# Kernel tuning notes

Hardware: AMD Instinct MI355X
Metric: run time of the kernel (lower is better)

Reference implementation:

```python
import jax, jax.numpy as jnp
import numpy as np

# dims: batch, seq, input_dim, excellence_dim, heads, n_experts, top_k
B, S, D, E, H, NE, K = 4, 256, 1024, 2048, 16, 4, 2
HD = E // H  # 128


def _ln(x, g, b, eps=1e-5):
    m = jnp.mean(x, -1, keepdims=True)
    v = jnp.mean((x - m) ** 2, -1, keepdims=True)
    return (x - m) / jnp.sqrt(v + eps) * g + b


def _mlp2(x, w1, b1, w2, b2):
    # Linear -> ReLU -> Linear (torch Linear convention: y = x @ W.T + b)
    return jnp.maximum(x @ w1.T + b1, 0.0) @ w2.T + b2


def _mha(h, in_w, in_b, out_w, out_b):
    # h: (B,S,E); fused qkv in_proj like nn.MultiheadAttention
    qkv = h @ in_w.T + in_b
    q, k, v = jnp.split(qkv, 3, axis=-1)
    sp = lambda t: t.reshape(B, S, H, HD).transpose(0, 2, 1, 3)  # (B,H,S,HD)
    q, k, v = sp(q), sp(k), sp(v)
    att = jax.nn.softmax(jnp.einsum('bhqd,bhkd->bhqk', q, k) / np.float32(np.sqrt(HD)), axis=-1)
    o = jnp.einsum('bhqk,bhkd->bhqd', att, v).transpose(0, 2, 1, 3).reshape(B, S, E)
    return o @ out_w.T + out_b


def _lstm(x, w_ih, w_hh, b_ih, b_hh):
    # single-layer LSTM, torch gate order i,f,g,o. x: (B,S,E)
    pre = jnp.einsum('bsd,gd->bsg', x, w_ih) + b_ih + b_hh  # (B,S,4E)

    def step(carry, p):
        h, c = carry
        g = p + h @ w_hh.T
        i, f, gg, o = jnp.split(g, 4, axis=-1)
        c = jax.nn.sigmoid(f) * c + jax.nn.sigmoid(i) * jnp.tanh(gg)
        h = jax.nn.sigmoid(o) * jnp.tanh(c)
        return (h, c), h

    h0 = jnp.zeros((x.shape[0], E), x.dtype)
    _, hs = jax.lax.scan(step, (h0, h0), pre.transpose(1, 0, 2))
    return hs.transpose(1, 0, 2)  # (B,S,E)


def _expert(p, x):
    h = _ln(_mlp2(x, p['enc_w1'], p['enc_b1'], p['enc_w2'], p['enc_b2']), p['enc_ln_g'], p['enc_ln_b'])
    a = _mha(h, p['attn_in_w'], p['attn_in_b'], p['attn_out_w'], p['attn_out_b'])
    m = _lstm(a, p['lstm_w_ih'], p['lstm_w_hh'], p['lstm_b_ih'], p['lstm_b_hh'])
    exc = jax.nn.sigmoid(_mlp2(m, p['exc_w1'], p['exc_b1'], p['exc_w2'], p['exc_b2']))
    opt = jnp.tanh(_mlp2(m, p['opt_w1'], p['opt_b1'], p['opt_w2'], p['opt_b2']))
    return _ln(_mlp2(exc * opt, p['dec_w1'], p['dec_b1'], p['dec_w2'], p['dec_b2']), p['dec_ln_g'], p['dec_ln_b'])


_PNAMES = ['enc_w1', 'enc_b1', 'enc_w2', 'enc_b2', 'enc_ln_g', 'enc_ln_b', 'attn_in_w', 'attn_in_b', 'attn_out_w', 'attn_out_b', 'lstm_w_ih', 'lstm_w_hh', 'lstm_b_ih', 'lstm_b_hh', 'exc_w1', 'exc_b1', 'exc_w2', 'exc_b2', 'opt_w1', 'opt_b1', 'opt_w2', 'opt_b2', 'dec_w1', 'dec_b1', 'dec_w2', 'dec_b2', 'dec_ln_g', 'dec_ln_b']


def _forward(x, gate_w, gate_b, *ep):
    p = dict(zip(_PNAMES, ep))  # each leaf has leading expert axis NE
    pooled = x.mean(axis=1)  # (B,D)
    probs = jax.nn.softmax(pooled @ gate_w + gate_b, axis=-1)  # (B,NE)
    vals, idx = jax.lax.top_k(probs, K)
    vals = vals / jnp.sum(vals, -1, keepdims=True)
    w = jnp.zeros((B, NE), x.dtype).at[jnp.arange(B)[:, None], idx].set(vals)
    outs = jax.vmap(lambda pe: _expert(pe, x))(p)  # (NE,B,S,D)
    return jnp.einsum('ebsd,be->bsd', outs, w)


def setup_inputs() -> dict:
    ks = iter(jax.random.split(jax.random.key(0), 40))
    w = lambda *s: jax.random.normal(next(ks), s, jnp.float32) * 0.02
    z = lambda *s: jnp.zeros(s, jnp.float32)
    o = lambda *s: jnp.ones(s, jnp.float32)
    return {
        'x': jax.random.normal(next(ks), (B, S, D), jnp.float32),
        'gate_w': w(D, NE), 'gate_b': z(NE),
        'enc_w1': w(NE, E, D), 'enc_b1': z(NE, E), 'enc_w2': w(NE, E, E), 'enc_b2': z(NE, E),
        'enc_ln_g': o(NE, E), 'enc_ln_b': z(NE, E),
        'attn_in_w': w(NE, 3 * E, E), 'attn_in_b': z(NE, 3 * E),
        'attn_out_w': w(NE, E, E), 'attn_out_b': z(NE, E),
        'lstm_w_ih': w(NE, 4 * E, E), 'lstm_w_hh': w(NE, 4 * E, E),
        'lstm_b_ih': z(NE, 4 * E), 'lstm_b_hh': z(NE, 4 * E),
        'exc_w1': w(NE, E, E), 'exc_b1': z(NE, E), 'exc_w2': w(NE, E, E), 'exc_b2': z(NE, E),
        'opt_w1': w(NE, E, E), 'opt_b1': z(NE, E), 'opt_w2': w(NE, E, E), 'opt_b2': z(NE, E),
        'dec_w1': w(NE, E, E), 'dec_b1': z(NE, E), 'dec_w2': w(NE, D, E), 'dec_b2': z(NE, D),
        'dec_ln_g': o(NE, D), 'dec_ln_b': z(NE, D),
    }


def reference(x, gate_w, gate_b, enc_w1, enc_b1, enc_w2, enc_b2, enc_ln_g, enc_ln_b, attn_in_w, attn_in_b, attn_out_w, attn_out_b, lstm_w_ih, lstm_w_hh, lstm_b_ih, lstm_b_hh, exc_w1, exc_b1, exc_w2, exc_b2, opt_w1, opt_b1, opt_w2, opt_b2, dec_w1, dec_b1, dec_w2, dec_b2, dec_ln_g, dec_ln_b):
    return _forward(x, gate_w, gate_b, enc_w1, enc_b1, enc_w2, enc_b2, enc_ln_g, enc_ln_b, attn_in_w, attn_in_b, attn_out_w, attn_out_b, lstm_w_ih, lstm_w_hh, lstm_b_ih, lstm_b_hh, exc_w1, exc_b1, exc_w2, exc_b2, opt_w1, opt_b1, opt_w2, opt_b2, dec_w1, dec_b1, dec_w2, dec_b2, dec_ln_g, dec_ln_b)
```

## Files before the change

kernel.cpp:

```cpp
#include <hip/hip_runtime.h>
#include <hip/hip_bf16.h>


typedef unsigned short u16;
typedef unsigned int u32;
typedef unsigned long long u64;
typedef __attribute__((ext_vector_type(8))) short short8;
typedef __attribute__((ext_vector_type(4))) float f32x4;

#define DEV static __device__ __forceinline__

DEV u16 f2bf(float f){ u32 u = __float_as_uint(f); u += 0x7fffu + ((u >> 16) & 1u); return (u16)(u >> 16); }
DEV float bf2f(u16 s){ return __uint_as_float(((u32)s) << 16); }
DEV u32 pk2(float a, float b){ return (u32)f2bf(a) | ((u32)f2bf(b) << 16); }
DEV float sigf(float x){ return 1.f / (1.f + __expf(-x)); }
DEV float sig_fast(float x){ return __builtin_amdgcn_rcpf(1.f + __expf(-x)); }
DEV float tanh_fast(float x){
  float ax = fabsf(x);
  float t = __expf(-2.f * ax);
  float r = (1.f - t) * __builtin_amdgcn_rcpf(1.f + t);
  return copysignf(r, x);
}

DEV void bred2(float& s, float& ss, float* red){
  #pragma unroll
  for (int o = 32; o; o >>= 1){ s += __shfl_xor(s, o); ss += __shfl_xor(ss, o); }
  int wv = threadIdx.x >> 6, ln = threadIdx.x & 63;
  if (ln == 0){ red[wv] = s; red[8 + wv] = ss; }
  __syncthreads();
  s = red[0] + red[1] + red[2] + red[3];
  ss = red[8] + red[9] + red[10] + red[11];
}

template<int BMODE, int SC, bool BIAS, bool RELU, bool SCALE>
__global__ void __launch_bounds__(256, 2) gemm_bt(
    const u16* __restrict__ A, const void* __restrict__ Bv,
    u16* __restrict__ C0, u16* __restrict__ C1, u16* __restrict__ C2,
    const float* __restrict__ bias,
    int N, int K, int lda, int ldb,
    long long sA, long long sB, long long sC, int sBias,
    int nbm, int nbn, float scale)
{
  __shared__ u16 As[128 * 40];
  __shared__ u16 Bs[128 * 40];
  int bid = blockIdx.x;
  int per = nbm * nbn;
  int batch = bid / per;
  int rem = bid - batch * per;
  int bm = rem % nbm, bn = rem / nbm;
  int t = threadIdx.x;
  int wave = t >> 6, lane = t & 63, fm = lane & 15, kg = lane >> 4;
  int wm = (wave >> 1) * 64, wn = (wave & 1) * 64;
  const u16* Ab = A + (size_t)batch * sA + (size_t)(bm * 128) * lda;
  f32x4 zero = {0.f, 0.f, 0.f, 0.f};
  f32x4 acc[4][4];
  #pragma unroll
  for (int i = 0; i < 4; ++i)
    #pragma unroll
    for (int j = 0; j < 4; ++j) acc[i][j] = zero;
  int nk = K >> 5;
  for (int ks = 0; ks < nk; ++ks){
    int k0 = ks << 5;
    #pragma unroll
    for (int it = 0; it < 2; ++it){
      int idx = it * 256 + t;
      int rr = idx >> 2, kc = idx & 3;
      *(uint4*)&As[rr * 40 + kc * 8] = *(const uint4*)(Ab + (size_t)rr * lda + k0 + kc * 8);
    }
    if constexpr (BMODE == 1){
      const u16* Bb = (const u16*)Bv + (size_t)batch * sB + (size_t)(bn * 128) * ldb;
      #pragma unroll
      for (int it = 0; it < 2; ++it){
        int idx = it * 256 + t;
        int rr = idx >> 2, kc = idx & 3;
        *(uint4*)&Bs[rr * 40 + kc * 8] = *(const uint4*)(Bb + (size_t)rr * ldb + k0 + kc * 8);
      }
    } else {
      int n = t >> 1, half = t & 1;
      const float* Bb = (const float*)Bv + (size_t)batch * sB + (size_t)(bn * 128 + n) * ldb + k0 + half * 16;
      float4 f0 = *(const float4*)(Bb);
      float4 f1 = *(const float4*)(Bb + 4);
      float4 f2 = *(const float4*)(Bb + 8);
      float4 f3 = *(const float4*)(Bb + 12);
      uint4 o0, o1;
      o0.x = pk2(f0.x, f0.y); o0.y = pk2(f0.z, f0.w);
      o0.z = pk2(f1.x, f1.y); o0.w = pk2(f1.z, f1.w);
      o1.x = pk2(f2.x, f2.y); o1.y = pk2(f2.z, f2.w);
      o1.z = pk2(f3.x, f3.y); o1.w = pk2(f3.z, f3.w);
      *(uint4*)&Bs[n * 40 + (half * 2 + 0) * 8] = o0;
      *(uint4*)&Bs[n * 40 + (half * 2 + 1) * 8] = o1;
    }
    __syncthreads();
    short8 afr[4], bfr[4];
    #pragma unroll
    for (int mi = 0; mi < 4; ++mi) afr[mi] = *(const short8*)&As[(wm + mi * 16 + fm) * 40 + kg * 8];
    #pragma unroll
    for (int ni = 0; ni < 4; ++ni) bfr[ni] = *(const short8*)&Bs[(wn + ni * 16 + fm) * 40 + kg * 8];
    #pragma unroll
    for (int mi = 0; mi < 4; ++mi)
      #pragma unroll
      for (int ni = 0; ni < 4; ++ni)
        acc[mi][ni] = __builtin_amdgcn_mfma_f32_16x16x32_bf16(afr[mi], bfr[ni], acc[mi][ni], 0, 0, 0);
    __syncthreads();
  }
  #pragma unroll
  for (int mi = 0; mi < 4; ++mi){
    #pragma unroll
    for (int ni = 0; ni < 4; ++ni){
      f32x4 v = acc[mi][ni];
      int gm0 = bm * 128 + wm + mi * 16 + kg * 4;
      int gn = bn * 128 + wn + ni * 16 + fm;
      float bv = 0.f;
      if constexpr (BIAS) bv = bias[(size_t)batch * sBias + gn];
      #pragma unroll
      for (int jj = 0; jj < 4; ++jj){
        float xv = v[jj];
        if constexpr (SCALE) xv *= scale;
        if constexpr (BIAS) xv += bv;
        if constexpr (RELU) xv = fmaxf(xv, 0.f);
        int gm = gm0 + jj;
        u16 ov = f2bf(xv);
        if constexpr (SC == 0){
          C0[(size_t)batch * sC + (size_t)gm * N + gn] = ov;
        } else if constexpr (SC == 1){
          int which = gn >> 11, hh = (gn >> 7) & 15, d = gn & 127;
          int b_ = gm >> 8, s_ = gm & 255;
          size_t hb = ((size_t)batch * 4 + b_) * 16 + hh;
          if (which == 0)      C0[(hb * 256 + s_) * 128 + d] = ov;
          else if (which == 1) C1[(hb * 256 + s_) * 128 + d] = ov;
          else                 C2[(hb * 128 + d) * 256 + s_] = ov;
        } else {
          int e_ = batch >> 6, b_ = (batch >> 4) & 3, hh = batch & 15;
          C0[(((size_t)e_ * 4 + b_) * 256 + gm) * 2048 + hh * 128 + gn] = ov;
        }
      }
    }
  }
}

__global__ void __launch_bounds__(256, 4) convert_x(const float* __restrict__ x, u16* __restrict__ xb){
  int idx = blockIdx.x * 256 + threadIdx.x;
  float4 a = *(const float4*)(x + (size_t)idx * 8);
  float4 b = *(const float4*)(x + (size_t)idx * 8 + 4);
  uint4 o;
  o.x = pk2(a.x, a.y); o.y = pk2(a.z, a.w); o.z = pk2(b.x, b.y); o.w = pk2(b.z, b.w);
  *(uint4*)(xb + (size_t)idx * 8) = o;
}

__global__ void __launch_bounds__(256, 4) comb_bias(const float* __restrict__ a, const float* __restrict__ b, float* __restrict__ o){
  int idx = blockIdx.x * 256 + threadIdx.x;
  float4 va = *(const float4*)(a + (size_t)idx * 4);
  float4 vb = *(const float4*)(b + (size_t)idx * 4);
  float4 r; r.x = va.x + vb.x; r.y = va.y + vb.y; r.z = va.z + vb.z; r.w = va.w + vb.w;
  *(float4*)(o + (size_t)idx * 4) = r;
}

__global__ void __launch_bounds__(256, 4) gate_pool(const float* __restrict__ x, float* __restrict__ pooled){
  int id = blockIdx.x * 256 + threadIdx.x;
  int b = id >> 10, d = id & 1023;
  const float* p = x + (size_t)b * 262144 + d;
  float s = 0.f;
  for (int si = 0; si < 256; ++si) s += p[si * 1024];
  pooled[id] = s * (1.f / 256.f);
}

__global__ void __launch_bounds__(256, 2) gate_top2(const float* __restrict__ pooled,
    const float* __restrict__ gw, const float* __restrict__ gb, float* __restrict__ wout)
{
  __shared__ float part[16][16];
  __shared__ float lg[4][4];
  int t = threadIdx.x;
  int pair = t >> 4, l = t & 15;
  int b = pair >> 2, e = pair & 3;
  float s = 0.f;
  for (int d = l; d < 1024; d += 16) s += pooled[b * 1024 + d] * gw[d * 4 + e];
  part[pair][l] = s;
  __syncthreads();
  if (t < 16){
    float v = 0.f;
    #pragma unroll
    for (int i = 0; i < 16; ++i) v += part[t][i];
    lg[t >> 2][t & 3] = v + gb[t & 3];
  }
  __syncthreads();
  if (t < 4){
    float p[4];
    float mx = -1e30f;
    for (int i = 0; i < 4; ++i) mx = fmaxf(mx, lg[t][i]);
    float sum = 0.f;
    for (int i = 0; i < 4; ++i){ p[i] = expf(lg[t][i] - mx); sum += p[i]; }
    for (int i = 0; i < 4; ++i) p[i] /= sum;
    int i1 = 0;
// ... 36 lines not shown
}

__global__ void __launch_bounds__(256, 4) softmax256(u16* __restrict__ sp){
  int row = blockIdx.x * 4 + (threadIdx.x >> 6);
  int ln = threadIdx.x & 63;
  u16* p = sp + (size_t)row * 256 + ln * 4;
  uint2 v = *(const uint2*)p;
  float f0 = bf2f(v.x & 0xffff), f1 = bf2f(v.x >> 16), f2 = bf2f(v.y & 0xffff), f3 = bf2f(v.y >> 16);
  float mx = fmaxf(fmaxf(f0, f1), fmaxf(f2, f3));
  #pragma unroll
  for (int o = 32; o; o >>= 1) mx = fmaxf(mx, __shfl_xor(mx, o));
  float e0 = __expf(f0 - mx), e1 = __expf(f1 - mx), e2 = __expf(f2 - mx), e3 = __expf(f3 - mx);
  float s = e0 + e1 + e2 + e3;
  #pragma unroll
  for (int o = 32; o; o >>= 1) s += __shfl_xor(s, o);
  float inv = 1.f / s;
  uint2 ov; ov.x = pk2(e0 * inv, e1 * inv); ov.y = pk2(e2 * inv, e3 * inv);
  *(uint2*)p = ov;
}

__global__ void __launch_bounds__(256, 2) wf_convert(const float* __restrict__ whh, u16* __restrict__ Wf){
  __shared__ float ls[16 * 260];
  int bid = blockIdx.x;
  int e = bid >> 12, nt = (bid >> 3) & 511, ktg = bid & 7;
  int t = threadIdx.x;
  const float* src = whh + ((size_t)e * 8192 + nt * 16) * 2048 + ktg * 256;
  #pragma unroll
  for (int it = 0; it < 4; ++it){
    int idx = it * 256 + t;
    int r = idx >> 6, f4 = (idx & 63) * 4;
    *(float4*)&ls[r * 260 + f4] = *(const float4*)(src + (size_t)r * 2048 + f4);
  }
  __syncthreads();
  #pragma unroll
  for (int it = 0; it < 2; ++it){
    int idx = it * 256 + t;
    int ktl = idx >> 6, lane = idx & 63;
    int r = lane & 15, kloc = ktl * 32 + (lane >> 4) * 8;
    float4 va = *(const float4*)&ls[r * 260 + kloc];
    float4 vb = *(const float4*)&ls[r * 260 + kloc + 4];
    uint4 o; o.x = pk2(va.x, va.y); o.y = pk2(va.z, va.w); o.z = pk2(vb.x, vb.y); o.w = pk2(vb.z, vb.w);
    size_t chunk = ((size_t)(e * 512 + nt) * 64 + (ktg * 8 + ktl)) * 64 + lane;
    *(uint4*)(Wf + chunk * 8) = o;
  }
}

__global__ void __launch_bounds__(512, 2) lstm_persist(
    const u16* __restrict__ Wf, const u16* __restrict__ pre,
    u16* hbuf,
    u16* __restrict__ mout,
    u32* flags)
{
  __shared__ u16 pinW[8 * 16 * 512];
  __shared__ u16 hA[8192];
  __shared__ float g_s[8][16][4];
  int blk = blockIdx.x;
  int e = blk >> 6, be = blk & 63;
  int jb = be * 32;
  int t = threadIdx.x;
  int wave = t >> 6, lane = t & 63;
  int fm = lane & 15, kg = lane >> 4;
  int gate = wave >> 1, half = wave & 1;
  int nt = gate * 128 + (jb >> 4) + half;
  const u16* wp = Wf + (((size_t)(e * 512 + nt) * 64) * 64 + lane) * 8;
  #pragma unroll
  for (int kt = 0; kt < 16; ++kt)
    *(uint4*)&pinW[(wave * 16 + kt) * 512 + lane * 8] = *(const uint4*)(wp + (size_t)kt * 512);
  short8 wreg[40];
  #pragma unroll
  for (int i = 0; i < 40; ++i)
    wreg[i] = *(const short8*)(wp + (size_t)(16 + i) * 512);
  const u16* wps = wp + (size_t)56 * 512;
  const u16* arow = &hA[kg * 32 + (fm & 3) * 8];
  int b_ = t >> 4, jp = t & 15;
  int w0 = jp >> 3, j0 = jp * 2, c0 = j0 & 15, c1 = c0 + 1;
  float creg0 = 0.f, creg1 = 0.f;
  u32* myflags = flags + e * 1024;
  size_t moutbase = ((size_t)(e * 4 + b_) * 256) * 2048 + jb + j0;
  for (int step = 0; step < 256; ++step){
    int par = step & 1;
    u32 pi = 0, pf = 0, pg = 0, po = 0;
    if (t < 64){
      size_t prebase = ((size_t)(e * 4 + b_) * 256 + step) * 8192 + jb + j0;
      pi = *(const u32*)(pre + prebase);
      pf = *(const u32*)(pre + prebase + 2048);
      pg = *(const u32*)(pre + prebase + 4096);
      po = *(const u32*)(pre + prebase + 6144);
    }
    const u16* hsrc = hbuf + par * 32768 + e * 8192;
    #pragma unroll
    for (int it = 0; it < 4; ++it){
      int c8 = it * 512 + t;
      int r = c8 >> 9, w4 = c8 & 511;
      u64 v = __hip_atomic_load((const u64*)(hsrc + r * 2048 + w4 * 4),
                                __ATOMIC_RELAXED, __HIP_MEMORY_SCOPE_AGENT);
      int di = (w4 >> 3) * 128 + ((w4 >> 1) & 3) * 32 + r * 8 + (w4 & 1) * 4;
      *(u64*)&hA[di] = v;
    }
    __syncthreads();
    short8 wtmp[8];
    #pragma unroll
    for (int i = 0; i < 8; ++i)
      wtmp[i] = *(const short8*)(wps + (size_t)i * 512);
    f32x4 acc[4];
    #pragma unroll
    for (int i = 0; i < 4; ++i) acc[i] = (f32x4){0.f, 0.f, 0.f, 0.f};
    #pragma unroll
    for (int kt = 0; kt < 16; ++kt){
      short8 a = *(const short8*)(arow + kt * 128);
      short8 b = *(const short8*)&pinW[(wave * 16 + kt) * 512 + lane * 8];
      acc[kt & 3] = __builtin_amdgcn_mfma_f32_16x16x32_bf16(a, b, acc[kt & 3], 0, 0, 0);
    }
    #pragma unroll
    for (int i = 0; i < 40; ++i){
      short8 a = *(const short8*)(arow + (16 + i) * 128);
      acc[i & 3] = __builtin_amdgcn_mfma_f32_16x16x32_bf16(a, wreg[i], acc[i & 3], 0, 0, 0);
    }
    #pragma unroll
    for (int i = 0; i < 8; ++i){
      short8 a = *(const short8*)(arow + (56 + i) * 128);
      acc[i & 3] = __builtin_amdgcn_mfma_f32_16x16x32_bf16(a, wtmp[i], acc[i & 3], 0, 0, 0);
    }
    f32x4 accs = (acc[0] + acc[1]) + (acc[2] + acc[3]);
    if (lane < 16){
      #pragma unroll
      for (int jj = 0; jj < 4; ++jj) g_s[wave][lane][jj] = accs[jj];
    }
    __syncthreads();
    if (t < 64){
      float gi0 = g_s[0 + w0][c0][b_] + bf2f(pi & 0xffff), gi1 = g_s[0 + w0][c1][b_] + bf2f(pi >> 16);
      float gf0 = g_s[2 + w0][c0][b_] + bf2f(pf & 0xffff), gf1 = g_s[2 + w0][c1][b_] + bf2f(pf >> 16);
      float gg0 = g_s[4 + w0][c0][b_] + bf2f(pg & 0xffff), gg1 = g_s[4 + w0][c1][b_] + bf2f(pg >> 16);
      float go0 = g_s[6 + w0][c0][b_] + bf2f(po & 0xffff), go1 = g_s[6 + w0][c1][b_] + bf2f(po >> 16);
      float c0v = sig_fast(gf0) * creg0 + sig_fast(gi0) * tanh_fast(gg0);
      float c1v = sig_fast(gf1) * creg1 + sig_fast(gi1) * tanh_fast(gg1);
      float h0 = sig_fast(go0) * tanh_fast(c0v);
      float h1 = sig_fast(go1) * tanh_fast(c1v);
      creg0 = c0v; creg1 = c1v;
      u32 hv = pk2(h0, h1);
      __hip_atomic_store((u32*)(hbuf + (par ^ 1) * 32768 + e * 8192 + b_ * 2048 + jb + j0), hv,
                         __ATOMIC_RELAXED, __HIP_MEMORY_SCOPE_AGENT);
      *(u32*)(mout + moutbase + (size_t)step * 2048) = hv;
    }
    __syncthreads();
    if (step < 255 && t < 64){
      if (t == 0)
        __hip_atomic_store(&myflags[be * 16], (u32)(step + 1), __ATOMIC_RELAXED, __HIP_MEMORY_SCOPE_AGENT);
      u32 fuel = 0;
      do {
        u32 f = __hip_atomic_load(&myflags[t * 16], __ATOMIC_RELAXED, __HIP_MEMORY_SCOPE_AGENT);
        if (!__any(f < (u32)(step + 1))) break;
        __builtin_amdgcn_s_sleep(1);
      } while (++fuel < (1u << 22));
    }
    __syncthreads();
  }
}

__global__ void __launch_bounds__(256, 4) eo_kernel(const u16* __restrict__ ep, const u16* __restrict__ op, u16* __restrict__ eo){
  int idx = blockIdx.x * 256 + threadIdx.x;
  uint4 ev = *(const uint4*)(ep + (size_t)idx * 8);
  uint4 ov = *(const uint4*)(op + (size_t)idx * 8);
  u32 e4[4] = {ev.x, ev.y, ev.z, ev.w};
  u32 o4[4] = {ov.x, ov.y, ov.z, ov.w};
  uint4 r;
  u32* rp = (u32*)&r;
  #pragma unroll
  for (int q = 0; q < 4; ++q){
    float a0 = sigf(bf2f(e4[q] & 0xffff)) * tanhf(bf2f(o4[q] & 0xffff));
    float a1 = sigf(bf2f(e4[q] >> 16)) * tanhf(bf2f(o4[q] >> 16));
    rp[q] = pk2(a0, a1);
  }
  *(uint4*)(eo + (size_t)idx * 8) = r;
}

__global__ void __launch_bounds__(256, 2) final_combine(const u16* __restrict__ decp, const float* __restrict__ wg,
    const float* __restrict__ gg, const float* __restrict__ bb, float* __restrict__ out)
{
  __shared__ float red[16];
  int tok = blockIdx.x;
  int b = tok >> 8;
  int t = threadIdx.x;
  float a0 = 0.f, a1 = 0.f, a2 = 0.f, a3 = 0.f;
  for (int e = 0; e < 4; ++e){
    const u16* p = decp + ((size_t)e * 1024 + tok) * 1024 + t * 4;
    uint2 v = *(const uint2*)p;
    float f0 = bf2f(v.x & 0xffff), f1 = bf2f(v.x >> 16), f2 = bf2f(v.y & 0xffff), f3 = bf2f(v.y >> 16);
    float s = f0 + f1 + f2 + f3;
    float ss = f0 * f0 + f1 * f1 + f2 * f2 + f3 * f3;
    bred2(s, ss, red);
    float mean = s * (1.f / 1024.f);
    float var = ss * (1.f / 1024.f) - mean * mean;
    float rstd = rsqrtf(var + 1e-5f);
    float we = wg[b * 4 + e];
    float4 gv = *(const float4*)(gg + (size_t)e * 1024 + t * 4);
    float4 bv = *(const float4*)(bb + (size_t)e * 1024 + t * 4);
    a0 += we * ((f0 - mean) * rstd * gv.x + bv.x);
    a1 += we * ((f1 - mean) * rstd * gv.y + bv.y);
    a2 += we * ((f2 - mean) * rstd * gv.z + bv.z);
    a3 += we * ((f3 - mean) * rstd * gv.w + bv.w);
    __syncthreads();
  }
  float4 r; r.x = a0; r.y = a1; r.z = a2; r.w = a3;
  *(float4*)(out + (size_t)tok * 1024 + t * 4) = r;
}

extern "C" void kernel_launch(void* const* d_in, const int* in_sizes, int n_in,
                              void* d_out, int out_size, void* d_ws, size_t ws_size,
                              hipStream_t stream)
{
  (void)in_sizes; (void)n_in; (void)out_size; (void)ws_size;
  const float* x        = (const float*)d_in[0];
  const float* gw       = (const float*)d_in[1];
  const float* gb       = (const float*)d_in[2];
  const float* enc_w1   = (const float*)d_in[3];
  const float* enc_b1   = (const float*)d_in[4];
  const float* enc_w2   = (const float*)d_in[5];
  const float* enc_b2   = (const float*)d_in[6];
  const float* enc_ln_g = (const float*)d_in[7];
  const float* enc_ln_b = (const float*)d_in[8];
  const float* ain_w    = (const float*)d_in[9];
  const float* ain_b    = (const float*)d_in[10];
  const float* aout_w   = (const float*)d_in[11];
  const float* aout_b   = (const float*)d_in[12];
  const float* w_ih     = (const float*)d_in[13];
  const float* w_hh     = (const float*)d_in[14];
  const float* b_ih     = (const float*)d_in[15];
  const float* b_hh     = (const float*)d_in[16];
  const float* exc_w1   = (const float*)d_in[17];
  const float* exc_b1   = (const float*)d_in[18];
  const float* exc_w2   = (const float*)d_in[19];
  const float* exc_b2   = (const float*)d_in[20];
  const float* opt_w1   = (const float*)d_in[21];
  const float* opt_b1   = (const float*)d_in[22];
  const float* opt_w2   = (const float*)d_in[23];
  const float* opt_b2   = (const float*)d_in[24];
  const float* dec_w1   = (const float*)d_in[25];
  const float* dec_b1   = (const float*)d_in[26];
  const float* dec_w2   = (const float*)d_in[27];
  const float* dec_b2   = (const float*)d_in[28];
  const float* dec_ln_g = (const float*)d_in[29];
  const float* dec_ln_b = (const float*)d_in[30];
  float* out = (float*)d_out;

  char* ws = (char*)d_ws;
  const size_t MB = 1ull << 20;
  u16* xbf  = (u16*)(ws);
  u16* h1   = (u16*)(ws + 2 * MB);
  u16* henc = (u16*)(ws + 18 * MB);
  u16* hbf  = (u16*)(ws + 34 * MB);
  u16* Qb   = (u16*)(ws + 2 * MB);
  u16* Kb   = (u16*)(ws + 18 * MB);
  u16* Vt   = (u16*)(ws + 50 * MB);
  u16* sp   = (u16*)(ws + 66 * MB);
  u16* abuf = (u16*)(ws + 2 * MB);
  u16* a_bf = (u16*)(ws + 18 * MB);
  u16* pre  = (u16*)(ws + 34 * MB);
  u16* Wf   = (u16*)(ws + 98 * MB);
  u16* mbuf = (u16*)(ws + 2 * MB);
  u16* t1   = (u16*)(ws + 18 * MB);
  u16* excp = (u16*)(ws + 34 * MB);
  u16* t2   = (u16*)(ws + 50 * MB);
  u16* optp = (u16*)(ws + 66 * MB);
  u16* eo   = (u16*)(ws + 82 * MB);
  u16* t3   = (u16*)(ws + 18 * MB);
  u16* decp = (u16*)(ws + 34 * MB);
  u16*   hbuf   = (u16*)(ws + 226 * MB);
  u32*   flags  = (u32*)(ws + 226 * MB + 128 * 1024);
  float* pooled = (float*)(ws + 226 * MB + 160 * 1024);
  float* wgate  = (float*)(ws + 226 * MB + 192 * 1024);
  float* cbias  = (float*)(ws + 226 * MB + 224 * 1024);

  hipMemsetAsync(hbuf, 0, 128 * 1024 + 16 * 1024, stream);

  convert_x<<<dim3(512), dim3(256), 0, stream>>>(x, xbf);
  wf_convert<<<dim3(16384), dim3(256), 0, stream>>>(w_hh, Wf);
  comb_bias<<<dim3(32), dim3(256), 0, stream>>>(b_ih, b_hh, cbias);
  gate_pool<<<dim3(16), dim3(256), 0, stream>>>(x, pooled);
  gate_top2<<<dim3(1), dim3(256), 0, stream>>>(pooled, gw, gb, wgate);

  gemm_bt<0, 0, true, true, false><<<dim3(512), dim3(256), 0, stream>>>(
      xbf, enc_w1, h1, nullptr, nullptr, enc_b1, 2048, 1024, 1024, 1024,
      0LL, 2048LL * 1024, 1024LL * 2048, 2048, 8, 16, 1.f);
  gemm_bt<0, 0, true, false, false><<<dim3(512), dim3(256), 0, stream>>>(
      h1, enc_w2, henc, nullptr, nullptr, enc_b2, 2048, 2048, 2048, 2048,
      1024LL * 2048, 2048LL * 2048, 1024LL * 2048, 2048, 8, 16, 1.f);
  ln2048<<<dim3(4096), dim3(256), 0, stream>>>(henc, hbf, enc_ln_g, enc_ln_b);

  gemm_bt<0, 1, true, false, false><<<dim3(1536), dim3(256), 0, stream>>>(
      hbf, ain_w, Qb, Kb, Vt, ain_b, 6144, 2048, 2048, 2048,
      1024LL * 2048, 6144LL * 2048, 0LL, 6144, 8, 48, 1.f);
  gemm_bt<1, 0, false, false, true><<<dim3(1024), dim3(256), 0, stream>>>(
      Qb, Kb, sp, nullptr, nullptr, nullptr, 256, 128, 128, 128,
      32768LL, 32768LL, 65536LL, 0, 2, 2, 0.08838834764831845f);
  softmax256<<<dim3(16384), dim3(256), 0, stream>>>(sp);
  gemm_bt<1, 2, false, false, false><<<dim3(512), dim3(256), 0, stream>>>(
      sp, Vt, abuf, nullptr, nullptr, nullptr, 128, 256, 256, 256,
      65536LL, 32768LL, 0LL, 0, 2, 1, 1.f);
  gemm_bt<0, 0, true, false, false><<<dim3(512), dim3(256), 0, stream>>>(
      abuf, aout_w, a_bf, nullptr, nullptr, aout_b, 2048, 2048, 2048, 2048,
      1024LL * 2048, 2048LL * 2048, 1024LL * 2048, 2048, 8, 16, 1.f);

  gemm_bt<0, 0, true, false, false><<<dim3(2048), dim3(256), 0, stream>>>(
      a_bf, w_ih, pre, nullptr, nullptr, cbias, 8192, 2048, 2048, 2048,
      1024LL * 2048, 8192LL * 2048, 1024LL * 8192, 8192, 8, 64, 1.f);
  lstm_persist<<<dim3(256), dim3(512), 0, stream>>>(Wf, pre, hbuf, mbuf, flags);

  gemm_bt<0, 0, true, true, false><<<dim3(512), dim3(256), 0, stream>>>(
      mbuf, exc_w1, t1, nullptr, nullptr, exc_b1, 2048, 2048, 2048, 2048,
      1024LL * 2048, 2048LL * 2048, 1024LL * 2048, 2048, 8, 16, 1.f);
  gemm_bt<0, 0, true, false, false><<<dim3(512), dim3(256), 0, stream>>>(
      t1, exc_w2, excp, nullptr, nullptr, exc_b2, 2048, 2048, 2048, 2048,
      1024LL * 2048, 2048LL * 2048, 1024LL * 2048, 2048, 8, 16, 1.f);
  gemm_bt<0, 0, true, true, false><<<dim3(512), dim3(256), 0, stream>>>(
      mbuf, opt_w1, t2, nullptr, nullptr, opt_b1, 2048, 2048, 2048, 2048,
      1024LL * 2048, 2048LL * 2048, 1024LL * 2048, 2048, 8, 16, 1.f);
  gemm_bt<0, 0, true, false, false><<<dim3(512), dim3(256), 0, stream>>>(
      t2, opt_w2, optp, nullptr, nullptr, opt_b2, 2048, 2048, 2048, 2048,
      1024LL * 2048, 2048LL * 2048, 1024LL * 2048, 2048, 8, 16, 1.f);
  eo_kernel<<<dim3(4096), dim3(256), 0, stream>>>(excp, optp, eo);
  gemm_bt<0, 0, true, true, false><<<dim3(512), dim3(256), 0, stream>>>(
      eo, dec_w1, t3, nullptr, nullptr, dec_b1, 2048, 2048, 2048, 2048,
      1024LL * 2048, 2048LL * 2048, 1024LL * 2048, 2048, 8, 16, 1.f);
  gemm_bt<0, 0, true, false, false><<<dim3(256), dim3(256), 0, stream>>>(
      t3, dec_w2, decp, nullptr, nullptr, dec_b2, 1024, 2048, 2048, 2048,
      1024LL * 2048, 1024LL * 2048, 1024LL * 1024, 1024, 8, 8, 1.f);

  final_combine<<<dim3(1024), dim3(256), 0, stream>>>(decp, wgate, dec_ln_g, dec_ln_b, out);
}
```

Before: 2.512 ms.

## Pre-convert weights to bf16 and load GEMM tiles with direct global-to-LDS copies

When the workspace is large enough, each fp32 weight matrix is first converted to bf16 in a scratch slot, and the GEMM then runs in its bf16 mode instead of converting B on the fly. The bf16 GEMM path now uses global_load_lds to copy A and B tiles straight into an unpadded LDS layout, with precomputed fragment offsets. The LSTM persistent kernel pads its h staging buffer row stride to 136 to reduce LDS bank conflicts, and its block-to-expert mapping is interleaved. This adds an extra conversion pass per weight, and the unpadded LDS layout may bring bank conflicts on fragment reads.

```diff
diff --git a/kernel.cpp b/kernel.cpp
--- a/kernel.cpp
+++ b/kernel.cpp
@@ -22,6 +22,11 @@
   return copysignf(r, x);
 }
 
+DEV void gld16(u16* lds, const u16* g){
+  __builtin_amdgcn_global_load_lds((const __attribute__((address_space(1))) u32*)g,
+                                   (__attribute__((address_space(3))) u32*)lds, 16, 0, 0);
+}
+
 DEV void bred2(float& s, float& ss, float* red){
   #pragma unroll
   for (int o = 32; o; o >>= 1){ s += __shfl_xor(s, o); ss += __shfl_xor(ss, o); }
@@ -41,8 +46,9 @@
     long long sA, long long sB, long long sC, int sBias,
     int nbm, int nbn, float scale)
 {
-  __shared__ u16 As[128 * 40];
-  __shared__ u16 Bs[128 * 40];
+  constexpr int LDW = (BMODE == 1) ? 32 : 40;
+  __shared__ u16 As[128 * LDW];
+  __shared__ u16 Bs[128 * LDW];
   int bid = blockIdx.x;
   int per = nbm * nbn;
   int batch = bid / per;
@@ -52,6 +58,16 @@
   int wave = t >> 6, lane = t & 63, fm = lane & 15, kg = lane >> 4;
   int wm = (wave >> 1) * 64, wn = (wave & 1) * 64;
   const u16* Ab = A + (size_t)batch * sA + (size_t)(bm * 128) * lda;
+  const u16* Bb16 = nullptr;
+  if constexpr (BMODE == 1)
+    Bb16 = (const u16*)Bv + (size_t)batch * sB + (size_t)(bn * 128) * ldb;
+  int aoff[4], boff[4];
+  if constexpr (BMODE == 1){
+    #pragma unroll
+    for (int mi = 0; mi < 4; ++mi) aoff[mi] = (wm + mi * 16 + fm) * 32 + kg * 8;
+    #pragma unroll
+    for (int ni = 0; ni < 4; ++ni) boff[ni] = (wn + ni * 16 + fm) * 32 + kg * 8;
+  }
   f32x4 zero = {0.f, 0.f, 0.f, 0.f};
   f32x4 acc[4][4];
   #pragma unroll
@@ -61,21 +77,22 @@
   int nk = K >> 5;
   for (int ks = 0; ks < nk; ++ks){
     int k0 = ks << 5;
-    #pragma unroll
-    for (int it = 0; it < 2; ++it){
-      int idx = it * 256 + t;
-      int rr = idx >> 2, kc = idx & 3;
-      *(uint4*)&As[rr * 40 + kc * 8] = *(const uint4*)(Ab + (size_t)rr * lda + k0 + kc * 8);
-    }
     if constexpr (BMODE == 1){
-      const u16* Bb = (const u16*)Bv + (size_t)batch * sB + (size_t)(bn * 128) * ldb;
+      #pragma unroll
+      for (int q = 0; q < 2; ++q){
+        int c = q * 256 + t;
+        int rr = c >> 2;
+        int kc8 = (c & 3) * 8;
+        gld16(&As[c * 8], Ab + (size_t)rr * lda + k0 + kc8);
+        gld16(&Bs[c * 8], Bb16 + (size_t)rr * ldb + k0 + kc8);
+      }
+    } else {
       #pragma unroll
       for (int it = 0; it < 2; ++it){
         int idx = it * 256 + t;
         int rr = idx >> 2, kc = idx & 3;
-        *(uint4*)&Bs[rr * 40 + kc * 8] = *(const uint4*)(Bb + (size_t)rr * ldb + k0 + kc * 8);
+        *(uint4*)&As[rr * LDW + kc * 8] = *(const uint4*)(Ab + (size_t)rr * lda + k0 + kc * 8);
       }
-    } else {
       int n = t >> 1, half = t & 1;
       const float* Bb = (const float*)Bv + (size_t)batch * sB + (size_t)(bn * 128 + n) * ldb + k0 + half * 16;
       float4 f0 = *(const float4*)(Bb);
@@ -87,15 +104,22 @@
       o0.z = pk2(f1.x, f1.y); o0.w = pk2(f1.z, f1.w);
       o1.x = pk2(f2.x, f2.y); o1.y = pk2(f2.z, f2.w);
       o1.z = pk2(f3.x, f3.y); o1.w = pk2(f3.z, f3.w);
-      *(uint4*)&Bs[n * 40 + (half * 2 + 0) * 8] = o0;
-      *(uint4*)&Bs[n * 40 + (half * 2 + 1) * 8] = o1;
+      *(uint4*)&Bs[n * LDW + (half * 2 + 0) * 8] = o0;
+      *(uint4*)&Bs[n * LDW + (half * 2 + 1) * 8] = o1;
     }
     __syncthreads();
     short8 afr[4], bfr[4];
-    #pragma unroll
-    for (int mi = 0; mi < 4; ++mi) afr[mi] = *(const short8*)&As[(wm + mi * 16 + fm) * 40 + kg * 8];
-    #pragma unroll
-    for (int ni = 0; ni < 4; ++ni) bfr[ni] = *(const short8*)&Bs[(wn + ni * 16 + fm) * 40 + kg * 8];
+    if constexpr (BMODE == 1){
+      #pragma unroll
+      for (int mi = 0; mi < 4; ++mi) afr[mi] = *(const short8*)&As[aoff[mi]];
+      #pragma unroll
+      for (int ni = 0; ni < 4; ++ni) bfr[ni] = *(const short8*)&Bs[boff[ni]];
+    } else {
+      #pragma unroll
+      for (int mi = 0; mi < 4; ++mi) afr[mi] = *(const short8*)&As[(wm + mi * 16 + fm) * LDW + kg * 8];
+      #pragma unroll
+      for (int ni = 0; ni < 4; ++ni) bfr[ni] = *(const short8*)&Bs[(wn + ni * 16 + fm) * LDW + kg * 8];
+    }
     #pragma unroll
     for (int mi = 0; mi < 4; ++mi)
       #pragma unroll
@@ -138,6 +162,17 @@
   }
 }
 
+__global__ void __launch_bounds__(256, 4) convf2b(const float* __restrict__ src, u16* __restrict__ dst, int n8){
+  int stride = gridDim.x * 256;
+  for (int i = blockIdx.x * 256 + threadIdx.x; i < n8; i += stride){
+    float4 a = *(const float4*)(src + (size_t)i * 8);
+    float4 b = *(const float4*)(src + (size_t)i * 8 + 4);
+    uint4 o;
+    o.x = pk2(a.x, a.y); o.y = pk2(a.z, a.w); o.z = pk2(b.x, b.y); o.w = pk2(b.z, b.w);
+    *(uint4*)(dst + (size_t)i * 8) = o;
+  }
+}
+
 __global__ void __launch_bounds__(256, 4) convert_x(const float* __restrict__ x, u16* __restrict__ xb){
   int idx = blockIdx.x * 256 + threadIdx.x;
   float4 a = *(const float4*)(x + (size_t)idx * 8);
@@ -280,10 +315,10 @@
     u32* flags)
 {
   __shared__ u16 pinW[8 * 16 * 512];
-  __shared__ u16 hA[8192];
+  __shared__ u16 hA[64 * 136];
   __shared__ float g_s[8][16][4];
   int blk = blockIdx.x;
-  int e = blk >> 6, be = blk & 63;
+  int e = blk & 3, be = blk >> 2;
   int jb = be * 32;
   int t = threadIdx.x;
   int wave = t >> 6, lane = t & 63;
@@ -322,7 +357,7 @@
       int r = c8 >> 9, w4 = c8 & 511;
       u64 v = __hip_atomic_load((const u64*)(hsrc + r * 2048 + w4 * 4),
                                 __ATOMIC_RELAXED, __HIP_MEMORY_SCOPE_AGENT);
-      int di = (w4 >> 3) * 128 + ((w4 >> 1) & 3) * 32 + r * 8 + (w4 & 1) * 4;
+      int di = (w4 >> 3) * 136 + ((w4 >> 1) & 3) * 32 + r * 8 + (w4 & 1) * 4;
       *(u64*)&hA[di] = v;
     }
     __syncthreads();
@@ -335,18 +370,18 @@
     for (int i = 0; i < 4; ++i) acc[i] = (f32x4){0.f, 0.f, 0.f, 0.f};
     #pragma unroll
     for (int kt = 0; kt < 16; ++kt){
-      short8 a = *(const short8*)(arow + kt * 128);
+      short8 a = *(const short8*)(arow + kt * 136);
       short8 b = *(const short8*)&pinW[(wave * 16 + kt) * 512 + lane * 8];
       acc[kt & 3] = __builtin_amdgcn_mfma_f32_16x16x32_bf16(a, b, acc[kt & 3], 0, 0, 0);
     }
     #pragma unroll
     for (int i = 0; i < 40; ++i){
-      short8 a = *(const short8*)(arow + (16 + i) * 128);
+      short8 a = *(const short8*)(arow + (16 + i) * 136);
       acc[i & 3] = __builtin_amdgcn_mfma_f32_16x16x32_bf16(a, wreg[i], acc[i & 3], 0, 0, 0);
     }
     #pragma unroll
     for (int i = 0; i < 8; ++i){
-      short8 a = *(const short8*)(arow + (56 + i) * 128);
+      short8 a = *(const short8*)(arow + (56 + i) * 136);
       acc[i & 3] = __builtin_amdgcn_mfma_f32_16x16x32_bf16(a, wtmp[i], acc[i & 3], 0, 0, 0);
     }
     f32x4 accs = (acc[0] + acc[1]) + (acc[2] + acc[3]);
@@ -437,7 +472,7 @@
                               void* d_out, int out_size, void* d_ws, size_t ws_size,
                               hipStream_t stream)
 {
-  (void)in_sizes; (void)n_in; (void)out_size; (void)ws_size;
+  (void)in_sizes; (void)n_in; (void)out_size;
   const float* x        = (const float*)d_in[0];
   const float* gw       = (const float*)d_in[1];
   const float* gb       = (const float*)d_in[2];
@@ -498,6 +533,8 @@
   float* pooled = (float*)(ws + 226 * MB + 160 * 1024);
   float* wgate  = (float*)(ws + 226 * MB + 192 * 1024);
   float* cbias  = (float*)(ws + 226 * MB + 224 * 1024);
+  u16*   wslot  = (u16*)(ws + 227 * MB);
+  const bool jit = ws_size >= 356ull * MB;
 
   hipMemsetAsync(hbuf, 0, 128 * 1024 + 16 * 1024, stream);
 
@@ -507,17 +544,37 @@
   gate_pool<<<dim3(16), dim3(256), 0, stream>>>(x, pooled);
   gate_top2<<<dim3(1), dim3(256), 0, stream>>>(pooled, gw, gb, wgate);
 
-  gemm_bt<0, 0, true, true, false><<<dim3(512), dim3(256), 0, stream>>>(
-      xbf, enc_w1, h1, nullptr, nullptr, enc_b1, 2048, 1024, 1024, 1024,
-      0LL, 2048LL * 1024, 1024LL * 2048, 2048, 8, 16, 1.f);
-  gemm_bt<0, 0, true, false, false><<<dim3(512), dim3(256), 0, stream>>>(
-      h1, enc_w2, henc, nullptr, nullptr, enc_b2, 2048, 2048, 2048, 2048,
-      1024LL * 2048, 2048LL * 2048, 1024LL * 2048, 2048, 8, 16, 1.f);
+  #define CONV(W, N8) convf2b<<<dim3(4096), dim3(256), 0, stream>>>(W, wslot, N8)
+
+  if (jit){
+    CONV(enc_w1, 1048576);
+    gemm_bt<1, 0, true, true, false><<<dim3(512), dim3(256), 0, stream>>>(
+        xbf, wslot, h1, nullptr, nullptr, enc_b1, 2048, 1024, 1024, 1024,
+        0LL, 2048LL * 1024, 1024LL * 2048, 2048, 8, 16, 1.f);
+    CONV(enc_w2, 2097152);
+    gemm_bt<1, 0, true, false, false><<<dim3(512), dim3(256), 0, stream>>>(
+        h1, wslot, henc, nullptr, nullptr, enc_b2, 2048, 2048, 2048, 2048,
+        1024LL * 2048, 2048LL * 2048, 1024LL * 2048, 2048, 8, 16, 1.f);
+  } else {
+    gemm_bt<0, 0, true, true, false><<<dim3(512), dim3(256), 0, stream>>>(
+        xbf, enc_w1, h1, nullptr, nullptr, enc_b1, 2048, 1024, 1024, 1024,
+        0LL, 2048LL * 1024, 1024LL * 2048, 2048, 8, 16, 1.f);
+    gemm_bt<0, 0, true, false, false><<<dim3(512), dim3(256), 0, stream>>>(
+        h1, enc_w2, henc, nullptr, nullptr, enc_b2, 2048, 2048, 2048, 2048,
+        1024LL * 2048, 2048LL * 2048, 1024LL * 2048, 2048, 8, 16, 1.f);
+  }
   ln2048<<<dim3(4096), dim3(256), 0, stream>>>(henc, hbf, enc_ln_g, enc_ln_b);
 
-  gemm_bt<0, 1, true, false, false><<<dim3(1536), dim3(256), 0, stream>>>(
-      hbf, ain_w, Qb, Kb, Vt, ain_b, 6144, 2048, 2048, 2048,
-      1024LL * 2048, 6144LL * 2048, 0LL, 6144, 8, 48, 1.f);
+  if (jit){
+    CONV(ain_w, 6291456);
+    gemm_bt<1, 1, true, false, false><<<dim3(1536), dim3(256), 0, stream>>>(
+        hbf, wslot, Qb, Kb, Vt, ain_b, 6144, 2048, 2048, 2048,
+        1024LL * 2048, 6144LL * 2048, 0LL, 6144, 8, 48, 1.f);
+  } else {
+    gemm_bt<0, 1, true, false, false><<<dim3(1536), dim3(256), 0, stream>>>(
+        hbf, ain_w, Qb, Kb, Vt, ain_b, 6144, 2048, 2048, 2048,
+        1024LL * 2048, 6144LL * 2048, 0LL, 6144, 8, 48, 1.f);
+  }
   gemm_bt<1, 0, false, false, true><<<dim3(1024), dim3(256), 0, stream>>>(
       Qb, Kb, sp, nullptr, nullptr, nullptr, 256, 128, 128, 128,
       32768LL, 32768LL, 65536LL, 0, 2, 2, 0.08838834764831845f);
@@ -525,34 +582,75 @@
   gemm_bt<1, 2, false, false, false><<<dim3(512), dim3(256), 0, stream>>>(
       sp, Vt, abuf, nullptr, nullptr, nullptr, 128, 256, 256, 256,
       65536LL, 32768LL, 0LL, 0, 2, 1, 1.f);
-  gemm_bt<0, 0, true, false, false><<<dim3(512), dim3(256), 0, stream>>>(
-      abuf, aout_w, a_bf, nullptr, nullptr, aout_b, 2048, 2048, 2048, 2048,
-      1024LL * 2048, 2048LL * 2048, 1024LL * 2048, 2048, 8, 16, 1.f);
-
-  gemm_bt<0, 0, true, false, false><<<dim3(2048), dim3(256), 0, stream>>>(
-      a_bf, w_ih, pre, nullptr, nullptr, cbias, 8192, 2048, 2048, 2048,
-      1024LL * 2048, 8192LL * 2048, 1024LL * 8192, 8192, 8, 64, 1.f);
+  if (jit){
+    CONV(aout_w, 2097152);
+    gemm_bt<1, 0, true, false, false><<<dim3(512), dim3(256), 0, stream>>>(
+        abuf, wslot, a_bf, nullptr, nullptr, aout_b, 2048, 2048, 2048, 2048,
+        1024LL * 2048, 2048LL * 2048, 1024LL * 2048, 2048, 8, 16, 1.f);
+    CONV(w_ih, 8388608);
+    gemm_bt<1, 0, true, false, false><<<dim3(2048), dim3(256), 0, stream>>>(
+        a_bf, wslot, pre, nullptr, nullptr, cbias, 8192, 2048, 2048, 2048,
+        1024LL * 2048, 8192LL * 2048, 1024LL * 8192, 8192, 8, 64, 1.f);
+  } else {
+    gemm_bt<0, 0, true, false, false><<<dim3(512), dim3(256), 0, stream>>>(
+        abuf, aout_w, a_bf, nullptr, nullptr, aout_b, 2048, 2048, 2048, 2048,
+        1024LL * 2048, 2048LL * 2048, 1024LL * 2048, 2048, 8, 16, 1.f);
+    gemm_bt<0, 0, true, false, false><<<dim3(2048), dim3(256), 0, stream>>>(
+        a_bf, w_ih, pre, nullptr, nullptr, cbias, 8192, 2048, 2048, 2048,
+        1024LL * 2048, 8192LL * 2048, 1024LL * 8192, 8192, 8, 64, 1.f);
+  }
   lstm_persist<<<dim3(256), dim3(512), 0, stream>>>(Wf, pre, hbuf, mbuf, flags);
 
-  gemm_bt<0, 0, true, true, false><<<dim3(512), dim3(256), 0, stream>>>(
-      mbuf, exc_w1, t1, nullptr, nullptr, exc_b1, 2048, 2048, 2048, 2048,
-      1024LL * 2048, 2048LL * 2048, 1024LL * 2048, 2048, 8, 16, 1.f);
-  gemm_bt<0, 0, true, false, false><<<dim3(512), dim3(256), 0, stream>>>(
-      t1, exc_w2, excp, nullptr, nullptr, exc_b2, 2048, 2048, 2048, 2048,
-      1024LL * 2048, 2048LL * 2048, 1024LL * 2048, 2048, 8, 16, 1.f);
-  gemm_bt<0, 0, true, true, false><<<dim3(512), dim3(256), 0, stream>>>(
-      mbuf, opt_w1, t2, nullptr, nullptr, opt_b1, 2048, 2048, 2048, 2048,
-      1024LL * 2048, 2048LL * 2048, 1024LL * 2048, 2048, 8, 16, 1.f);
-  gemm_bt<0, 0, true, false, false><<<dim3(512), dim3(256), 0, stream>>>(
-      t2, opt_w2, optp, nullptr, nullptr, opt_b2, 2048, 2048, 2048, 2048,
-      1024LL * 2048, 2048LL * 2048, 1024LL * 2048, 2048, 8, 16, 1.f);
+  if (jit){
+    CONV(exc_w1, 2097152);
+    gemm_bt<1, 0, true, true, false><<<dim3(512), dim3(256), 0, stream>>>(
+        mbuf, wslot, t1, nullptr, nullptr, exc_b1, 2048, 2048, 2048, 2048,
+        1024LL * 2048, 2048LL * 2048, 1024LL * 2048, 2048, 8, 16, 1.f);
+    CONV(exc_w2, 2097152);
+    gemm_bt<1, 0, true, false, false><<<dim3(512), dim3(256), 0, stream>>>(
+        t1, wslot, excp, nullptr, nullptr, exc_b2, 2048, 2048, 2048, 2048,
+        1024LL * 2048, 2048LL * 2048, 1024LL * 2048, 2048, 8, 16, 1.f);
+    CONV(opt_w1, 2097152);
+    gemm_bt<1, 0, true, true, false><<<dim3(512), dim3(256), 0, stream>>>(
+        mbuf, wslot, t2, nullptr, nullptr, opt_b1, 2048, 2048, 2048, 2048,
+        1024LL * 2048, 2048LL * 2048, 1024LL * 2048, 2048, 8, 16, 1.f);
+    CONV(opt_w2, 2097152);
+    gemm_bt<1, 0, true, false, false><<<dim3(512), dim3(256), 0, stream>>>(
+        t2, wslot, optp, nullptr, nullptr, opt_b2, 2048, 2048, 2048, 2048,
+        1024LL * 2048, 2048LL * 2048, 1024LL * 2048, 2048, 8, 16, 1.f);
+  } else {
+    gemm_bt<0, 0, true, true, false><<<dim3(512), dim3(256), 0, stream>>>(
+        mbuf, exc_w1, t1, nullptr, nullptr, exc_b1, 2048, 2048, 2048, 2048,
+        1024LL * 2048, 2048LL * 2048, 1024LL * 2048, 2048, 8, 16, 1.f);
+    gemm_bt<0, 0, true, false, false><<<dim3(512), dim3(256), 0, stream>>>(
+        t1, exc_w2, excp, nullptr, nullptr, exc_b2, 2048, 2048, 2048, 2048,
+        1024LL * 2048, 2048LL * 2048, 1024LL * 2048, 2048, 8, 16, 1.f);
+    gemm_bt<0, 0, true, true, false><<<dim3(512), dim3(256), 0, stream>>>(
+        mbuf, opt_w1, t2, nullptr, nullptr, opt_b1, 2048, 2048, 2048, 2048,
+        1024LL * 2048, 2048LL * 2048, 1024LL * 2048, 2048, 8, 16, 1.f);
+    gemm_bt<0, 0, true, false, false><<<dim3(512), dim3(256), 0, stream>>>(
+        t2, opt_w2, optp, nullptr, nullptr, opt_b2, 2048, 2048, 2048, 2048,
+        1024LL * 2048, 2048LL * 2048, 1024LL * 2048, 2048, 8, 16, 1.f);
+  }
   eo_kernel<<<dim3(4096), dim3(256), 0, stream>>>(excp, optp, eo);
-  gemm_bt<0, 0, true, true, false><<<dim3(512), dim3(256), 0, stream>>>(
-      eo, dec_w1, t3, nullptr, nullptr, dec_b1, 2048, 2048, 2048, 2048,
-      1024LL * 2048, 2048LL * 2048, 1024LL * 2048, 2048, 8, 16, 1.f);
-  gemm_bt<0, 0, true, false, false><<<dim3(256), dim3(256), 0, stream>>>(
-      t3, dec_w2, decp, nullptr, nullptr, dec_b2, 1024, 2048, 2048, 2048,
-      1024LL * 2048, 1024LL * 2048, 1024LL * 1024, 1024, 8, 8, 1.f);
+  if (jit){
+    CONV(dec_w1, 2097152);
+    gemm_bt<1, 0, true, true, false><<<dim3(512), dim3(256), 0, stream>>>(
+        eo, wslot, t3, nullptr, nullptr, dec_b1, 2048, 2048, 2048, 2048,
+        1024LL * 2048, 2048LL * 2048, 1024LL * 2048, 2048, 8, 16, 1.f);
+    CONV(dec_w2, 1048576);
+    gemm_bt<1, 0, true, false, false><<<dim3(256), dim3(256), 0, stream>>>(
+        t3, wslot, decp, nullptr, nullptr, dec_b2, 1024, 2048, 2048, 2048,
+        1024LL * 2048, 1024LL * 2048, 1024LL * 1024, 1024, 8, 8, 1.f);
+  } else {
+    gemm_bt<0, 0, true, true, false><<<dim3(512), dim3(256), 0, stream>>>(
+        eo, dec_w1, t3, nullptr, nullptr, dec_b1, 2048, 2048, 2048, 2048,
+        1024LL * 2048, 2048LL * 2048, 1024LL * 2048, 2048, 8, 16, 1.f);
+    gemm_bt<0, 0, true, false, false><<<dim3(256), dim3(256), 0, stream>>>(
+        t3, dec_w2, decp, nullptr, nullptr, dec_b2, 1024, 2048, 2048, 2048,
+        1024LL * 2048, 1024LL * 2048, 1024LL * 1024, 1024, 8, 8, 1.f);
+  }
+  #undef CONV
 
   final_combine<<<dim3(1024), dim3(256), 0, stream>>>(decp, wgate, dec_ln_g, dec_ln_b, out);
 }
```

Measured after the change: 2.205 ms. 1.14x faster.

## Load GEMM A tiles directly into LDS and pad LSTM hidden-state buffer

Applied to the files above, without the earlier changes.

The GEMM kernel now stages A tiles, and B tiles in the bf16-B mode, with global_load_lds direct-to-LDS transfers instead of register round-trips. This requires an unpadded 32-element row stride in LDS, which may bring back bank conflicts on the MFMA fragment reads. In the persistent LSTM kernel, the hidden-state LDS tile gets a padded 136-element stride to reduce bank conflicts. Blocks are also interleaved across experts rather than grouped by expert. The GEMM call sites switch to a template mode value that still takes the fp32-B conversion path.

```diff
diff --git a/kernel.cpp b/kernel.cpp
--- a/kernel.cpp
+++ b/kernel.cpp
@@ -22,6 +22,11 @@
   return copysignf(r, x);
 }
 
+DEV void gld16(u16* lds, const u16* g){
+  __builtin_amdgcn_global_load_lds((const __attribute__((address_space(1))) u32*)g,
+                                   (__attribute__((address_space(3))) u32*)lds, 16, 0, 0);
+}
+
 DEV void bred2(float& s, float& ss, float* red){
   #pragma unroll
   for (int o = 32; o; o >>= 1){ s += __shfl_xor(s, o); ss += __shfl_xor(ss, o); }
@@ -41,8 +46,9 @@
     long long sA, long long sB, long long sC, int sBias,
     int nbm, int nbn, float scale)
 {
-  __shared__ u16 As[128 * 40];
-  __shared__ u16 Bs[128 * 40];
+  constexpr int LDB_ = (BMODE == 1) ? 32 : 40;
+  __shared__ u16 As[128 * 32];
+  __shared__ u16 Bs[128 * LDB_];
   int bid = blockIdx.x;
   int per = nbm * nbn;
   int batch = bid / per;
@@ -52,6 +58,14 @@
   int wave = t >> 6, lane = t & 63, fm = lane & 15, kg = lane >> 4;
   int wm = (wave >> 1) * 64, wn = (wave & 1) * 64;
   const u16* Ab = A + (size_t)batch * sA + (size_t)(bm * 128) * lda;
+  const u16* Bb16 = nullptr;
+  if constexpr (BMODE == 1)
+    Bb16 = (const u16*)Bv + (size_t)batch * sB + (size_t)(bn * 128) * ldb;
+  int aoff[4], boff[4];
+  #pragma unroll
+  for (int mi = 0; mi < 4; ++mi) aoff[mi] = (wm + mi * 16 + fm) * 32 + kg * 8;
+  #pragma unroll
+  for (int ni = 0; ni < 4; ++ni) boff[ni] = (wn + ni * 16 + fm) * LDB_ + kg * 8;
   f32x4 zero = {0.f, 0.f, 0.f, 0.f};
   f32x4 acc[4][4];
   #pragma unroll
@@ -61,21 +75,23 @@
   int nk = K >> 5;
   for (int ks = 0; ks < nk; ++ks){
     int k0 = ks << 5;
-    #pragma unroll
-    for (int it = 0; it < 2; ++it){
-      int idx = it * 256 + t;
-      int rr = idx >> 2, kc = idx & 3;
-      *(uint4*)&As[rr * 40 + kc * 8] = *(const uint4*)(Ab + (size_t)rr * lda + k0 + kc * 8);
-    }
     if constexpr (BMODE == 1){
-      const u16* Bb = (const u16*)Bv + (size_t)batch * sB + (size_t)(bn * 128) * ldb;
       #pragma unroll
-      for (int it = 0; it < 2; ++it){
-        int idx = it * 256 + t;
-        int rr = idx >> 2, kc = idx & 3;
-        *(uint4*)&Bs[rr * 40 + kc * 8] = *(const uint4*)(Bb + (size_t)rr * ldb + k0 + kc * 8);
+      for (int q = 0; q < 2; ++q){
+        int c = q * 256 + t;
+        int rr = c >> 2;
+        int kc8 = (c & 3) * 8;
+        gld16(&As[c * 8], Ab + (size_t)rr * lda + k0 + kc8);
+        gld16(&Bs[c * 8], Bb16 + (size_t)rr * ldb + k0 + kc8);
       }
     } else {
+      #pragma unroll
+      for (int q = 0; q < 2; ++q){
+        int c = q * 256 + t;
+        int rr = c >> 2;
+        int kc8 = (c & 3) * 8;
+        gld16(&As[c * 8], Ab + (size_t)rr * lda + k0 + kc8);
+      }
       int n = t >> 1, half = t & 1;
       const float* Bb = (const float*)Bv + (size_t)batch * sB + (size_t)(bn * 128 + n) * ldb + k0 + half * 16;
       float4 f0 = *(const float4*)(Bb);
@@ -93,9 +109,9 @@
     __syncthreads();
     short8 afr[4], bfr[4];
     #pragma unroll
-    for (int mi = 0; mi < 4; ++mi) afr[mi] = *(const short8*)&As[(wm + mi * 16 + fm) * 40 + kg * 8];
-    #pragma unroll
-    for (int ni = 0; ni < 4; ++ni) bfr[ni] = *(const short8*)&Bs[(wn + ni * 16 + fm) * 40 + kg * 8];
+    for (int mi = 0; mi < 4; ++mi) afr[mi] = *(const short8*)&As[aoff[mi]];
+    #pragma unroll
+    for (int ni = 0; ni < 4; ++ni) bfr[ni] = *(const short8*)&Bs[boff[ni]];
     #pragma unroll
     for (int mi = 0; mi < 4; ++mi)
       #pragma unroll
@@ -280,10 +296,10 @@
     u32* flags)
 {
   __shared__ u16 pinW[8 * 16 * 512];
-  __shared__ u16 hA[8192];
+  __shared__ u16 hA[64 * 136];
   __shared__ float g_s[8][16][4];
   int blk = blockIdx.x;
-  int e = blk >> 6, be = blk & 63;
+  int e = blk & 3, be = blk >> 2;
   int jb = be * 32;
   int t = threadIdx.x;
   int wave = t >> 6, lane = t & 63;
@@ -322,7 +338,7 @@
       int r = c8 >> 9, w4 = c8 & 511;
       u64 v = __hip_atomic_load((const u64*)(hsrc + r * 2048 + w4 * 4),
                                 __ATOMIC_RELAXED, __HIP_MEMORY_SCOPE_AGENT);
-      int di = (w4 >> 3) * 128 + ((w4 >> 1) & 3) * 32 + r * 8 + (w4 & 1) * 4;
+      int di = (w4 >> 3) * 136 + ((w4 >> 1) & 3) * 32 + r * 8 + (w4 & 1) * 4;
       *(u64*)&hA[di] = v;
     }
     __syncthreads();
@@ -335,18 +351,18 @@
     for (int i = 0; i < 4; ++i) acc[i] = (f32x4){0.f, 0.f, 0.f, 0.f};
     #pragma unroll
     for (int kt = 0; kt < 16; ++kt){
-      short8 a = *(const short8*)(arow + kt * 128);
+      short8 a = *(const short8*)(arow + kt * 136);
       short8 b = *(const short8*)&pinW[(wave * 16 + kt) * 512 + lane * 8];
       acc[kt & 3] = __builtin_amdgcn_mfma_f32_16x16x32_bf16(a, b, acc[kt & 3], 0, 0, 0);
     }
     #pragma unroll
     for (int i = 0; i < 40; ++i){
-      short8 a = *(const short8*)(arow + (16 + i) * 128);
+      short8 a = *(const short8*)(arow + (16 + i) * 136);
       acc[i & 3] = __builtin_amdgcn_mfma_f32_16x16x32_bf16(a, wreg[i], acc[i & 3], 0, 0, 0);
     }
     #pragma unroll
     for (int i = 0; i < 8; ++i){
-      short8 a = *(const short8*)(arow + (56 + i) * 128);
+      short8 a = *(const short8*)(arow + (56 + i) * 136);
       acc[i & 3] = __builtin_amdgcn_mfma_f32_16x16x32_bf16(a, wtmp[i], acc[i & 3], 0, 0, 0);
     }
     f32x4 accs = (acc[0] + acc[1]) + (acc[2] + acc[3]);
@@ -507,15 +523,15 @@
   gate_pool<<<dim3(16), dim3(256), 0, stream>>>(x, pooled);
   gate_top2<<<dim3(1), dim3(256), 0, stream>>>(pooled, gw, gb, wgate);
 
-  gemm_bt<0, 0, true, true, false><<<dim3(512), dim3(256), 0, stream>>>(
+  gemm_bt<2, 0, true, true, false><<<dim3(512), dim3(256), 0, stream>>>(
       xbf, enc_w1, h1, nullptr, nullptr, enc_b1, 2048, 1024, 1024, 1024,
       0LL, 2048LL * 1024, 1024LL * 2048, 2048, 8, 16, 1.f);
-  gemm_bt<0, 0, true, false, false><<<dim3(512), dim3(256), 0, stream>>>(
+  gemm_bt<2, 0, true, false, false><<<dim3(512), dim3(256), 0, stream>>>(
       h1, enc_w2, henc, nullptr, nullptr, enc_b2, 2048, 2048, 2048, 2048,
       1024LL * 2048, 2048LL * 2048, 1024LL * 2048, 2048, 8, 16, 1.f);
   ln2048<<<dim3(4096), dim3(256), 0, stream>>>(henc, hbf, enc_ln_g, enc_ln_b);
 
-  gemm_bt<0, 1, true, false, false><<<dim3(1536), dim3(256), 0, stream>>>(
+  gemm_bt<2, 1, true, false, false><<<dim3(1536), dim3(256), 0, stream>>>(
       hbf, ain_w, Qb, Kb, Vt, ain_b, 6144, 2048, 2048, 2048,
       1024LL * 2048, 6144LL * 2048, 0LL, 6144, 8, 48, 1.f);
   gemm_bt<1, 0, false, false, true><<<dim3(1024), dim3(256), 0, stream>>>(
@@ -525,32 +541,32 @@
   gemm_bt<1, 2, false, false, false><<<dim3(512), dim3(256), 0, stream>>>(
       sp, Vt, abuf, nullptr, nullptr, nullptr, 128, 256, 256, 256,
       65536LL, 32768LL, 0LL, 0, 2, 1, 1.f);
-  gemm_bt<0, 0, true, false, false><<<dim3(512), dim3(256), 0, stream>>>(
+  gemm_bt<2, 0, true, false, false><<<dim3(512), dim3(256), 0, stream>>>(
       abuf, aout_w, a_bf, nullptr, nullptr, aout_b, 2048, 2048, 2048, 2048,
       1024LL * 2048, 2048LL * 2048, 1024LL * 2048, 2048, 8, 16, 1.f);
 
-  gemm_bt<0, 0, true, false, false><<<dim3(2048), dim3(256), 0, stream>>>(
+  gemm_bt<2, 0, true, false, false><<<dim3(2048), dim3(256), 0, stream>>>(
       a_bf, w_ih, pre, nullptr, nullptr, cbias, 8192, 2048, 2048, 2048,
       1024LL * 2048, 8192LL * 2048, 1024LL * 8192, 8192, 8, 64, 1.f);
   lstm_persist<<<dim3(256), dim3(512), 0, stream>>>(Wf, pre, hbuf, mbuf, flags);
 
-  gemm_bt<0, 0, true, true, false><<<dim3(512), dim3(256), 0, stream>>>(
+  gemm_bt<2, 0, true, true, false><<<dim3(512), dim3(256), 0, stream>>>(
       mbuf, exc_w1, t1, nullptr, nullptr, exc_b1, 2048, 2048, 2048, 2048,
       1024LL * 2048, 2048LL * 2048, 1024LL * 2048, 2048, 8, 16, 1.f);
-  gemm_bt<0, 0, true, false, false><<<dim3(512), dim3(256), 0, stream>>>(
+  gemm_bt<2, 0, true, false, false><<<dim3(512), dim3(256), 0, stream>>>(
       t1, exc_w2, excp, nullptr, nullptr, exc_b2, 2048, 2048, 2048, 2048,
       1024LL * 2048, 2048LL * 2048, 1024LL * 2048, 2048, 8, 16, 1.f);
-  gemm_bt<0, 0, true, true, false><<<dim3(512), dim3(256), 0, stream>>>(
+  gemm_bt<2, 0, true, true, false><<<dim3(512), dim3(256), 0, stream>>>(
       mbuf, opt_w1, t2, nullptr, nullptr, opt_b1, 2048, 2048, 2048, 2048,
       1024LL * 2048, 2048LL * 2048, 1024LL * 2048, 2048, 8, 16, 1.f);
-  gemm_bt<0, 0, true, false, false><<<dim3(512), dim3(256), 0, stream>>>(
+  gemm_bt<2, 0, true, false, false><<<dim3(512), dim3(256), 0, stream>>>(
       t2, opt_w2, optp, nullptr, nullptr, opt_b2, 2048, 2048, 2048, 2048,
       1024LL * 2048, 2048LL * 2048, 1024LL * 2048, 2048, 8, 16, 1.f);
   eo_kernel<<<dim3(4096), dim3(256), 0, stream>>>(excp, optp, eo);
-  gemm_bt<0, 0, true, true, false><<<dim3(512), dim3(256), 0, stream>>>(
+  gemm_bt<2, 0, true, true, false><<<dim3(512), dim3(256), 0, stream>>>(
       eo, dec_w1, t3, nullptr, nullptr, dec_b1, 2048, 2048, 2048, 2048,
       1024LL * 2048, 2048LL * 2048, 1024LL * 2048, 2048, 8, 16, 1.f);
-  gemm_bt<0, 0, true, false, false><<<dim3(256), dim3(256), 0, stream>>>(
+  gemm_bt<2, 0, true, false, false><<<dim3(256), dim3(256), 0, stream>>>(
       t3, dec_w2, decp, nullptr, nullptr, dec_b2, 1024, 2048, 2048, 2048,
       1024LL * 2048, 1024LL * 2048, 1024LL * 1024, 1024, 8, 8, 1.f);
 
```

Result: no change. 2.483 ms (-1.2%).
